# Optimization experiments

Measured on AMD Instinct MI355X. Metric: run time of the kernel, lower is better.

The kernel has to match this reference:

```python
import jax, jax.numpy as jnp
import numpy as np

B, S, J, L, E, H, NI, NT = 8, 32, 4, 32, 500, 500, 5000, 48


def _lstm_scan(x, h0, c0, Wi, Wh, b):
    # x: [T, ..., E]; torch LSTM gate order i,f,g,o
    def step(carry, xt):
        h, c = carry
        z = xt @ Wi.T + h @ Wh.T + b
        i, f, g, o = jnp.split(z, 4, axis=-1)
        c = jax.nn.sigmoid(f) * c + jax.nn.sigmoid(i) * jnp.tanh(g)
        h = jax.nn.sigmoid(o) * jnp.tanh(c)
        return (h, c), h
    (h, c), hs = jax.lax.scan(step, (h0, c0), x)
    return hs, (h, c)


def setup_inputs() -> dict:
    key = jax.random.key(0)
    ks = jax.random.split(key, 24)
    p = lambda k, shp: jax.random.normal(k, shp, jnp.float32) * 0.05
    t = jnp.arange(S)
    return dict(
        item_vectors=jax.random.randint(ks[0], (B, S), 0, NI),
        sequence_tim=jax.random.randint(ks[1], (B, S), 0, NT),
        dilated_idx=jax.random.randint(ks[2], (B, S), 0, S) % jnp.maximum(t, 1)[None, :],
        hist_items=jax.random.randint(ks[3], (B, J, L), 0, NI),
        hist_tims=jax.random.randint(ks[4], (B, J, L), 0, NT),
        mask=jnp.ones((B, S), jnp.float32),
        tim_sim=jax.random.uniform(ks[5], (NT, NT)),
        poi_dist=jax.random.uniform(ks[6], (NI, NI)) + 0.1,
        emb_W=p(ks[7], (NI, E)),
        lstm_Wi=p(ks[8], (4 * H, E)), lstm_Wh=p(ks[9], (4 * H, H)), lstm_b=jnp.zeros((4 * H,)),
        hist_Wi=p(ks[10], (4 * H, E)), hist_Wh=p(ks[11], (4 * H, H)), hist_b=jnp.zeros((4 * H,)),
        dil_Wi=p(ks[12], (4 * H, E)), dil_Wh=p(ks[13], (4 * H, H)), dil_b=jnp.zeros((4 * H,)),
        lin1_W=p(ks[14], (H, H)), lin1_b=jnp.zeros((H,)),
        lin_W=p(ks[15], (NI, 2 * H)), lin_b=jnp.zeros((NI,)),
    )


def _fwd(item_vectors, sequence_tim, dilated_idx, hist_items, hist_tims, mask,
         tim_sim, poi_dist, emb_W, lstm_Wi, lstm_Wh, lstm_b, hist_Wi, hist_Wh,
         hist_b, dil_Wi, dil_Wh, dil_b, lin1_W, lin1_b, lin_W, lin_b):
    items = emb_W[item_vectors]                                  # [B,S,E]
    hs, _ = _lstm_scan(items.transpose(1, 0, 2), jnp.zeros((B, H)), jnp.zeros((B, H)),
                       lstm_Wi, lstm_Wh, lstm_b)
    out = hs.transpose(1, 0, 2)                                  # [B,S,H]

    def dilated_one(xb, idx):
        # dilated LSTMCell: prev state gathered from data-dependent index (zeros at t=0)
        def step(carry, inp):
            Hs, Cs = carry
            t, it, xt = inp
            ph = jnp.where(t == 0, jnp.zeros((H,)), Hs[it])
            pc = jnp.where(t == 0, jnp.zeros((H,)), Cs[it])
            z = xt @ dil_Wi.T + ph @ dil_Wh.T + dil_b
            i, f, g, o = jnp.split(z, 4)
            c = jax.nn.sigmoid(f) * pc + jax.nn.sigmoid(i) * jnp.tanh(g)
            h = jax.nn.sigmoid(o) * jnp.tanh(c)
            return (Hs.at[t].set(h), Cs.at[t].set(c)), None
        (Hs, _), _ = jax.lax.scan(step, (jnp.zeros((S, H)), jnp.zeros((S, H))),
                                  (jnp.arange(S), idx, xb))
        return Hs
    out_hie = jax.vmap(dilated_one)(items, dilated_idx)          # [B,S,H]

    # train-branch session representation: masked mean, same at every step
    denom = jnp.sum(mask, axis=1, keepdims=True)
    pooled = jnp.sum(out * mask[:, :, None], axis=1) / denom     # [B,H]
    csr = jnp.broadcast_to(pooled[:, None, :], (B, S - 1, H))

    def hist_one(items_j, tims_j, timid, poiid, csr_b, out_b):
        jac_rows = tim_sim[timid]                                # [S-1,NT]
        dist_rows = poi_dist[poiid]                              # [S-1,NI]
        def sess_step(carry, inp):
            h2, c2 = carry
            itms, tms = inp
            he, (h2, c2) = _lstm_scan(emb_W[itms], h2, c2, hist_Wi, hist_Wh, hist_b)
            w = jax.nn.softmax(jac_rows[:, tms], axis=1)         # [S-1,L]
            sess_rep = w @ he                                    # [S-1,H]
            avg_d = jnp.mean(dist_rows[:, itms], axis=1)         # [S-1]
            return (h2, c2), (sess_rep, avg_d)
        _, (sess, avgd) = jax.lax.scan(sess_step, (jnp.zeros((H,)), jnp.zeros((H,))),
                                       (items_j, tims_j))
        sess_t = sess.transpose(1, 0, 2)                         # [S-1,J,H]
        avgd_t = avgd.T                                          # [S-1,J]
        sims = jax.nn.softmax(jnp.einsum('sjh,sh->sj', sess_t, csr_b), axis=1)
        out_y = jax.nn.selu(jnp.einsum('sj,sjh->sh', sims, sess_t) @ lin1_W.T + lin1_b)
        layer2 = 0.5 * out_y + 0.5 * out_b[:S - 1]
        l2s = jax.nn.softmax(jnp.einsum('sjh,sh->sj', sess_t, layer2) / avgd_t, axis=1)
        ol2 = jnp.einsum('sj,sjh->sh', l2s, sess_t)              # [S-1,H]
        return jnp.concatenate([ol2, jnp.zeros((1, H))], axis=0)  # pad to [S,H]

    y = jax.nn.selu(jax.vmap(hist_one)(hist_items, hist_tims, sequence_tim[:, :S - 1],
                                       item_vectors[:, :S - 1], csr, out))
    out_mix = 0.5 * (jax.nn.selu(out) + jax.nn.selu(out_hie))
    logits = jnp.concatenate([y, out_mix], axis=2) @ lin_W.T + lin_b
    return jax.nn.log_softmax(logits, axis=-1)


def reference(item_vectors, sequence_tim, dilated_idx, hist_items, hist_tims, mask,
              tim_sim, poi_dist, emb_W, lstm_Wi, lstm_Wh, lstm_b, hist_Wi, hist_Wh,
              hist_b, dil_Wi, dil_Wh, dil_b, lin1_W, lin1_b, lin_W, lin_b):
    return _fwd(item_vectors, sequence_tim, dilated_idx, hist_items, hist_tims, mask,
                tim_sim, poi_dist, emb_W, lstm_Wi, lstm_Wh, lstm_b, hist_Wi, hist_Wh,
                hist_b, dil_Wi, dil_Wh, dil_b, lin1_W, lin1_b, lin_W, lin_b)
```

## Files before the change

### kernel.cpp

```cpp
#include <hip/hip_runtime.h>
#include <hip/hip_bf16.h>
#include <math.h>

#define B_ 8
#define S_ 32
#define J_ 4
#define L_ 32
#define E_ 500
#define H_ 500
#define NI_ 5000
#define NT_ 48
#define G4_ 2000

#define PZH_ 2.0f
#define PZC_ 1e30f

typedef unsigned long long ull;

__device__ __forceinline__ float sigm(float x) { return 1.f / (1.f + expf(-x)); }
__device__ __forceinline__ float seluf(float x) {
    const float sc = 1.0507009873554805f, al = 1.6732632423543772f;
    return x > 0.f ? sc * x : sc * al * (expf(x) - 1.f);
}
__device__ __forceinline__ float cohload(const float* p) {
    return __hip_atomic_load(p, __ATOMIC_RELAXED, __HIP_MEMORY_SCOPE_AGENT);
}
__device__ __forceinline__ ull cohload64(const ull* p) {
    return __hip_atomic_load(p, __ATOMIC_RELAXED, __HIP_MEMORY_SCOPE_AGENT);
}
__device__ __forceinline__ void cohstore(float* p, float v) {
    __hip_atomic_store(p, v, __ATOMIC_RELAXED, __HIP_MEMORY_SCOPE_AGENT);
}

__global__ __launch_bounds__(256) void k_poison(float* __restrict__ outm,
                                                float* __restrict__ outh,
                                                float* __restrict__ csg,
                                                float* __restrict__ he) {
    int i = blockIdx.x * 256 + threadIdx.x;
    if (i < 128000) { outm[i] = PZH_; outh[i] = PZH_; csg[i] = PZC_; }
    if (i < 512000) he[i] = PZH_;
}

__global__ __launch_bounds__(128) void k_embed(const int* __restrict__ itemv,
                                               const int* __restrict__ histi,
                                               const float* __restrict__ embW,
                                               float* __restrict__ items,
                                               float* __restrict__ histemb) {
    int row = blockIdx.x;
    int id;
    float* dst;
    if (row < 256) { id = itemv[row]; dst = items + (size_t)row * E_; }
    else           { int rr = row - 256; id = histi[rr]; dst = histemb + (size_t)rr * E_; }
    const float4* s = (const float4*)(embW + (size_t)id * E_);
    float4* d = (float4*)dst;
    if (threadIdx.x < 125) d[threadIdx.x] = s[threadIdx.x];
}

#define TBM 64
#define TBN 64
#define TBK 16
__global__ __launch_bounds__(256) void k_gemm_bt(const float* __restrict__ A,
                                                 const float* __restrict__ Bm,
                                                 const float* __restrict__ bias,
                                                 float* __restrict__ C,
                                                 int M, int N, int K) {
    __shared__ float As[TBK][TBM + 1];
    __shared__ float Bs[TBK][TBN + 1];
    const int tid = threadIdx.x;
    const int tx = tid & 15, ty = tid >> 4;
    const int row0 = blockIdx.y * TBM, col0 = blockIdx.x * TBN;
    float acc[4][4] = {};
    for (int k0 = 0; k0 < K; k0 += TBK) {
#pragma unroll
        for (int i = 0; i < 4; ++i) {
            int e = tid + i * 256;
            int kk = e & 15, m = e >> 4;
            int gk = k0 + kk;
            float va = 0.f, vb = 0.f;
            int gm = row0 + m, gn = col0 + m;
            if (gk < K) {
                if (gm < M) va = A[(size_t)gm * K + gk];
                if (gn < N) vb = Bm[(size_t)gn * K + gk];
            }
            As[kk][m] = va;
            Bs[kk][m] = vb;
        }
        __syncthreads();
#pragma unroll
        for (int kk = 0; kk < TBK; ++kk) {
            float a[4], bb[4];
#pragma unroll
            for (int i = 0; i < 4; ++i) a[i] = As[kk][ty * 4 + i];
#pragma unroll
            for (int i = 0; i < 4; ++i) bb[i] = Bs[kk][tx * 4 + i];
#pragma unroll
            for (int i = 0; i < 4; ++i)
#pragma unroll
                for (int j = 0; j < 4; ++j) acc[i][j] += a[i] * bb[j];
        }
        __syncthreads();
    }
#pragma unroll
    for (int i = 0; i < 4; ++i) {
        int gm = row0 + ty * 4 + i;
        if (gm >= M) continue;
#pragma unroll
        for (int j = 0; j < 4; ++j) {
            int gn = col0 + tx * 4 + j;
            if (gn < N) C[(size_t)gm * N + gn] = acc[i][j] + (bias ? bias[gn] : 0.f);
        }
    }
}

__global__ __launch_bounds__(256) void k_rec10(
    const float* __restrict__ xwm, const float* __restrict__ Whm,
    const float* __restrict__ xwd, const float* __restrict__ Whd,
    const int* __restrict__ dilidx,
    const float* __restrict__ xwh, const float* __restrict__ Whh,
    float* __restrict__ outm, float* __restrict__ outh,
    float* __restrict__ csg, float* __restrict__ he) {
    __shared__ __align__(16) float4 h_s4[125];
    __shared__ float z_s[256];
    const int tid = threadIdx.x;
    const int bid = blockIdx.x;
    const int x = bid & 7, ii = bid >> 3;
    int role, b, blk;
    if (x < 4)      { role = 2; b = x * 2 + (ii >> 4);       blk = ii & 15; }
    else if (x < 6) { role = 0; b = (x - 4) * 4 + (ii >> 3); blk = ii & 7;  }
    else            { role = 1; b = (x - 6) * 4 + (ii >> 3); blk = ii & 7;  }

    const int hpbb   = (role == 2) ? 32 : 63;
    const int r0     = blk * hpbb;
    const int hpb    = min(hpbb, 500 - r0);
    const int C      = 4 * hpb;
    const int nsteps = (role == 2) ? 128 : 32;

    const float* Wh = (role == 0) ? Whm : (role == 1) ? Whd : Whh;
    const float* xw = (role == 0) ? xwm : (role == 1) ? xwd : xwh;

    int colg = 0;
    if (tid < C) {
        int gate = tid / hpb;
        int ri = tid - gate * hpb;
        colg = gate * 500 + r0 + ri;
    }
    const float4* wp4 = (const float4*)(Wh + (size_t)colg * 500);

    float c_reg = 0.f;

    for (int t = 0; t < nsteps; ++t) {
        float acc = 0.f;
        if (tid < C) acc = xw[((size_t)(b * nsteps + t)) * G4_ + colg];

        float pc_r = 0.f;
        if (t > 0) {
            const float* hrow;
            if (role == 0)      hrow = outm + ((size_t)(b * S_ + (t - 1))) * H_;
            else if (role == 2) hrow = he + ((size_t)(b * 128 + (t - 1))) * H_;
            else { int it = dilidx[b * S_ + t];
                   hrow = outh + ((size_t)(b * S_ + it)) * H_; }
            if (tid < 125) {
                const ull* p = (const ull*)(hrow + tid * 4);
                union { ull u[2]; float4 f; float fs[4]; } uf;
                while (true) {
                    uf.u[0] = cohload64(p);
                    uf.u[1] = cohload64(p + 1);
                    if (uf.fs[0] != PZH_ && uf.fs[1] != PZH_ &&
                        uf.fs[2] != PZH_ && uf.fs[3] != PZH_) break;
                    __builtin_amdgcn_s_sleep(1);
                }
                h_s4[tid] = uf.f;
            }
            if (role == 1 && tid < hpb) {
                int it = dilidx[b * S_ + t];
                const float* pp = &csg[((size_t)(b * S_ + it)) * H_ + r0 + tid];
                do { pc_r = cohload(pp); } while (pc_r == PZC_);
            }
            __syncthreads();

            if (tid < C) {
                float s0 = 0.f, s1 = 0.f, s2 = 0.f, s3 = 0.f;
#pragma unroll 2
                for (int k4 = 0; k4 < 124; k4 += 4) {
                    float4 w0 = wp4[k4],     h0 = h_s4[k4];
                    float4 w1 = wp4[k4 + 1], h1 = h_s4[k4 + 1];
                    float4 w2 = wp4[k4 + 2], h2 = h_s4[k4 + 2];
                    float4 w3 = wp4[k4 + 3], h3 = h_s4[k4 + 3];
                    s0 += w0.x * h0.x + w0.y * h0.y + w0.z * h0.z + w0.w * h0.w;
                    s1 += w1.x * h1.x + w1.y * h1.y + w1.z * h1.z + w1.w * h1.w;
                    s2 += w2.x * h2.x + w2.y * h2.y + w2.z * h2.z + w2.w * h2.w;
                    s3 += w3.x * h3.x + w3.y * h3.y + w3.z * h3.z + w3.w * h3.w;
                }
                float4 wt = wp4[124], ht = h_s4[124];
                s0 += wt.x * ht.x + wt.y * ht.y + wt.z * ht.z + wt.w * ht.w;
                acc += (s0 + s1) + (s2 + s3);
            }
        }
        z_s[tid] = acc;
        __syncthreads();

        if (tid < hpb) {
            float zi = z_s[tid];
            float zf = z_s[tid + hpb];
            float zg = z_s[tid + 2 * hpb];
            float zo = z_s[tid + 3 * hpb];
            float pc = (role == 1) ? pc_r : c_reg;
            float cc = sigm(zf) * pc + sigm(zi) * tanhf(zg);
            float hh = sigm(zo) * tanhf(cc);
            c_reg = cc;
            int r = r0 + tid;
            if (role == 0) {
                cohstore(&outm[((size_t)(b * S_ + t)) * H_ + r], hh);
            } else if (role == 2) {
                cohstore(&he[((size_t)(b * 128 + t)) * H_ + r], hh);
            } else {
                cohstore(&outh[((size_t)(b * S_ + t)) * H_ + r], hh);
                cohstore(&csg[((size_t)(b * S_ + t)) * H_ + r], cc);
            }
        }
        __syncthreads();
    }
}

__global__ __launch_bounds__(512) void k_pool(const float* __restrict__ outm,
                                              const float* __restrict__ mask,
                                              float* __restrict__ pooled) {
    int b = blockIdx.x, tid = threadIdx.x;
    if (tid >= 500) return;
    float acc = 0.f, den = 0.f;
    for (int s = 0; s < S_; ++s) {
        float mk = mask[b * S_ + s];
        acc += outm[((size_t)(b * S_ + s)) * H_ + tid] * mk;
        den += mk;
    }
    pooled[b * H_ + tid] = acc / den;
}

__global__ __launch_bounds__(512) void k_sess(const int* __restrict__ seqtim,
                                              const int* __restrict__ itemv,
                                              const int* __restrict__ histt,
                                              const int* __restrict__ histi,
                                              const float* __restrict__ timsim,
                                              const float* __restrict__ poid,
                                              const float* __restrict__ he,
                                              float* __restrict__ sess,
                                              float* __restrict__ avgd) {
    int bi = blockIdx.x;
    int s = bi % 31;
    int tmpv = bi / 31;
    int j = tmpv & 3, b = tmpv >> 2;
    __shared__ float w[L_];
    __shared__ float pd[L_];
    __shared__ float stats[1];
    int tid = threadIdx.x;
    int st = seqtim[b * S_ + s];
    if (tid < L_) {
        int ht = histt[(b * J_ + j) * L_ + tid];
        w[tid] = timsim[st * NT_ + ht];
    }
    if (tid >= 64 && tid < 64 + L_) {
        int l = tid - 64;
        int iv = itemv[b * S_ + s];
        pd[l] = poid[(size_t)iv * NI_ + histi[(b * J_ + j) * L_ + l]];
    }
    __syncthreads();
    if (tid == 64) {
        float a = 0.f;
        for (int l = 0; l < L_; ++l) a += pd[l];
        avgd[(b * J_ + j) * 31 + s] = a * (1.f / 32.f);
    }
    if (tid == 0) {
        float m = -1e30f;
        for (int l = 0; l < L_; ++l) m = fmaxf(m, w[l]);
        float sm = 0.f;
        for (int l = 0; l < L_; ++l) { float e = expf(w[l] - m); w[l] = e; sm += e; }
        stats[0] = 1.f / sm;
    }
    __syncthreads();
    if (tid < 500) {
        float inv = stats[0];
        float acc = 0.f;
        const float* hp = he + ((size_t)(b * J_ * L_ + j * L_)) * H_ + tid;
        for (int l = 0; l < L_; ++l) acc += w[l] * inv * hp[(size_t)l * H_];
        sess[((size_t)((b * J_ + j) * 31 + s)) * H_ + tid] = acc;
    }
}

__global__ __launch_bounds__(512) void k_att1(const float* __restrict__ sess,
                                              const float* __restrict__ pooled,
                                              float* __restrict__ att1) {
    int bi = blockIdx.x;
    int s = bi % 31, b = bi / 31;
    __shared__ float vec[H_];
    __shared__ float part[512];
    int tid = threadIdx.x;
    if (tid < 500) vec[tid] = pooled[b * H_ + tid];
    __syncthreads();
    int j = tid >> 7, i = tid & 127;
    const float* sp = sess + ((size_t)((b * J_ + j) * 31 + s)) * H_;
    float acc = 0.f;
    for (int h = i; h < H_; h += 128) acc += sp[h] * vec[h];
    part[tid] = acc;
    __syncthreads();
    for (int off = 64; off > 0; off >>= 1) {
        if (i < off) part[tid] += part[tid + off];
        __syncthreads();
    }
    float d0 = part[0], d1 = part[128], d2 = part[256], d3 = part[384];
    float m = fmaxf(fmaxf(d0, d1), fmaxf(d2, d3));
    float e0 = expf(d0 - m), e1 = expf(d1 - m), e2 = expf(d2 - m), e3 = expf(d3 - m);
    float inv = 1.f / (e0 + e1 + e2 + e3);
    if (tid < 500) {
        const float* s0 = sess + ((size_t)(b * J_ * 31 + s)) * H_ + tid;
        const size_t js = (size_t)31 * H_;
        float r = e0 * inv * s0[0] + e1 * inv * s0[js] + e2 * inv * s0[2 * js] + e3 * inv * s0[3 * js];
        att1[((size_t)(b * 31 + s)) * H_ + tid] = r;
    }
}

__global__ __launch_bounds__(512) void k_att2(const float* __restrict__ sess,
                                              const float* __restrict__ outy,
                                              const float* __restrict__ outm,
                                              const float* __restrict__ avgd,
                                              float* __restrict__ X) {
    int bi = blockIdx.x;
    int s = bi % 31, b = bi / 31;
    __shared__ float vec[H_];
    __shared__ float part[512];
    int tid = threadIdx.x;
    if (tid < 500)
        vec[tid] = 0.5f * seluf(outy[((size_t)(b * 31 + s)) * H_ + tid]) +
                   0.5f * outm[((size_t)(b * S_ + s)) * H_ + tid];
    __syncthreads();
    int j = tid >> 7, i = tid & 127;
    const float* sp = sess + ((size_t)((b * J_ + j) * 31 + s)) * H_;
    float acc = 0.f;
    for (int h = i; h < H_; h += 128) acc += sp[h] * vec[h];
    part[tid] = acc;
    __syncthreads();
    for (int off = 64; off > 0; off >>= 1) {
        if (i < off) part[tid] += part[tid + off];
        __syncthreads();
    }
    float d0 = part[0]   / avgd[(b * J_ + 0) * 31 + s];
    float d1 = part[128] / avgd[(b * J_ + 1) * 31 + s];
    float d2 = part[256] / avgd[(b * J_ + 2) * 31 + s];
    float d3 = part[384] / avgd[(b * J_ + 3) * 31 + s];
    float m = fmaxf(fmaxf(d0, d1), fmaxf(d2, d3));
    float e0 = expf(d0 - m), e1 = expf(d1 - m), e2 = expf(d2 - m), e3 = expf(d3 - m);
    float inv = 1.f / (e0 + e1 + e2 + e3);
    if (tid < 500) {
        const float* s0 = sess + ((size_t)(b * J_ * 31 + s)) * H_ + tid;
        const size_t js = (size_t)31 * H_;
        float r = e0 * inv * s0[0] + e1 * inv * s0[js] + e2 * inv * s0[2 * js] + e3 * inv * s0[3 * js];
        X[((size_t)(b * S_ + s)) * 1000 + tid] = seluf(r);
    }
}

__global__ __launch_bounds__(512) void k_mix(const float* __restrict__ outm,
                                             const float* __restrict__ outh,
                                             float* __restrict__ X) {
    int bs = blockIdx.x;
    int tid = threadIdx.x;
    if (tid >= 500) return;
    size_t idx = (size_t)bs * H_ + tid;
    float om = 0.5f * (seluf(outm[idx]) + seluf(outh[idx]));
    X[(size_t)bs * 1000 + 500 + tid] = om;
    if ((bs & (S_ - 1)) == S_ - 1) X[(size_t)bs * 1000 + tid] = 0.f;
}

__global__ __launch_bounds__(512) void k_lsm(float* __restrict__ out) {
    int row = blockIdx.x, tid = threadIdx.x;
    float* p = out + (size_t)row * NI_;
    __shared__ float red[512];
    float m = -1e30f;
    for (int i = tid; i < NI_; i += 512) m = fmaxf(m, p[i]);
    red[tid] = m;
    __syncthreads();
    for (int off = 256; off > 0; off >>= 1) {
        if (tid < off) red[tid] = fmaxf(red[tid], red[tid + off]);
        __syncthreads();
    }
    m = red[0];
    __syncthreads();
    float sm = 0.f;
    for (int i = tid; i < NI_; i += 512) sm += expf(p[i] - m);
    red[tid] = sm;
    __syncthreads();
    for (int off = 256; off > 0; off >>= 1) {
        if (tid < off) red[tid] += red[tid + off];
        __syncthreads();
    }
    float lse = m + logf(red[0]);
    __syncthreads();
    for (int i = tid; i < NI_; i += 512) p[i] -= lse;
}

extern "C" void kernel_launch(void* const* d_in, const int* in_sizes, int n_in,
                              void* d_out, int out_size, void* d_ws, size_t ws_size,
                              hipStream_t stream) {
    const int* item_vectors = (const int*)d_in[0];
    const int* sequence_tim = (const int*)d_in[1];
    const int* dilated_idx  = (const int*)d_in[2];
    const int* hist_items   = (const int*)d_in[3];
    const int* hist_tims    = (const int*)d_in[4];
    const float* mask       = (const float*)d_in[5];
    const float* tim_sim    = (const float*)d_in[6];
    const float* poi_dist   = (const float*)d_in[7];
    const float* emb_W      = (const float*)d_in[8];
    const float* lstm_Wi    = (const float*)d_in[9];
    const float* lstm_Wh    = (const float*)d_in[10];
    const float* lstm_b     = (const float*)d_in[11];
    const float* hist_Wi    = (const float*)d_in[12];
    const float* hist_Wh    = (const float*)d_in[13];
    const float* hist_b     = (const float*)d_in[14];
    const float* dil_Wi     = (const float*)d_in[15];
    const float* dil_Wh     = (const float*)d_in[16];
    const float* dil_b      = (const float*)d_in[17];
    const float* lin1_W     = (const float*)d_in[18];
    const float* lin1_b     = (const float*)d_in[19];
    const float* lin_W      = (const float*)d_in[20];
    const float* lin_b      = (const float*)d_in[21];
    float* out = (float*)d_out;
    float* ws  = (float*)d_ws;

    float* items   = ws + 0;
    float* histemb = ws + 128000;
    float* xwm     = ws + 640000;
    float* xwd     = ws + 1152000;
    float* xwh     = ws + 1664000;
    float* outm    = ws + 3712000;
    float* outh    = ws + 3840000;
    float* csg     = ws + 3968000;
    float* he      = ws + 4096000;
    float* pooled  = ws + 4608000;
    float* sess    = ws + 4612000;
    float* avgd    = ws + 5108000;
    float* att1    = ws + 5108992;
    float* outy    = ws + 5232992;
    float* Xbuf    = ws + 5356992;

    k_poison<<<dim3(2000), dim3(256), 0, stream>>>(outm, outh, csg, he);
    k_embed<<<dim3(1280), dim3(128), 0, stream>>>(item_vectors, hist_items, emb_W, items, histemb);

    k_gemm_bt<<<dim3(32, 4), dim3(256), 0, stream>>>(items, lstm_Wi, lstm_b, xwm, 256, G4_, E_);
    k_gemm_bt<<<dim3(32, 4), dim3(256), 0, stream>>>(items, dil_Wi, dil_b, xwd, 256, G4_, E_);
    k_gemm_bt<<<dim3(32, 16), dim3(256), 0, stream>>>(histemb, hist_Wi, hist_b, xwh, 1024, G4_, E_);

    k_rec10<<<dim3(256), dim3(256), 0, stream>>>(
        xwm, lstm_Wh, xwd, dil_Wh, dilated_idx, xwh, hist_Wh,
        outm, outh, csg, he);

    k_pool<<<dim3(B_), dim3(512), 0, stream>>>(outm, mask, pooled);
    k_sess<<<dim3(B_ * J_ * 31), dim3(512), 0, stream>>>(sequence_tim, item_vectors, hist_tims,
                                                         hist_items, tim_sim, poi_dist, he, sess, avgd);
    k_att1<<<dim3(B_ * 31), dim3(512), 0, stream>>>(sess, pooled, att1);
    k_gemm_bt<<<dim3(8, 4), dim3(256), 0, stream>>>(att1, lin1_W, lin1_b, outy, 248, H_, H_);
    k_att2<<<dim3(B_ * 31), dim3(512), 0, stream>>>(sess, outy, outm, avgd, Xbuf);
    k_mix<<<dim3(B_ * S_), dim3(512), 0, stream>>>(outm, outh, Xbuf);

    k_gemm_bt<<<dim3(79, 4), dim3(256), 0, stream>>>(Xbuf, lin_W, lin_b, out, 256, NI_, 1000);
    k_lsm<<<dim3(256), dim3(512), 0, stream>>>(out);
}
```

Baseline: 1.892 ms.

## Fuse embedding gather into input GEMMs, replace poison kernel with memset, merge mix into att2

Swaps the poison kernel for a single hipMemsetAsync that fills the sync buffers with a 0x7F7F7F7F bit pattern, and the recurrence now spin-waits on that bit pattern. Folds the embedding gather into a single three-way batched input-projection GEMM launch, so the items/histemb buffers are never materialized. Also folds the mix kernel into the att2 kernel, which now covers all 32 steps. Together these cut launch count and intermediate memory traffic. In exchange the GEMM does an indirect embedding load per A element, and blocks in the z=0/1 slices whose rows lie past 256 exit early.

```diff
diff --git a/kernel.cpp b/kernel.cpp
--- a/kernel.cpp
+++ b/kernel.cpp
@@ -12,8 +12,7 @@
 #define NT_ 48
 #define G4_ 2000
 
-#define PZH_ 2.0f
-#define PZC_ 1e30f
+#define PZBITS_ 0x7F7F7F7Fu
 
 typedef unsigned long long ull;
 
@@ -32,33 +31,72 @@
     __hip_atomic_store(p, v, __ATOMIC_RELAXED, __HIP_MEMORY_SCOPE_AGENT);
 }
 
-__global__ __launch_bounds__(256) void k_poison(float* __restrict__ outm,
-                                                float* __restrict__ outh,
-                                                float* __restrict__ csg,
-                                                float* __restrict__ he) {
-    int i = blockIdx.x * 256 + threadIdx.x;
-    if (i < 128000) { outm[i] = PZH_; outh[i] = PZH_; csg[i] = PZC_; }
-    if (i < 512000) he[i] = PZH_;
-}
-
-__global__ __launch_bounds__(128) void k_embed(const int* __restrict__ itemv,
-                                               const int* __restrict__ histi,
-                                               const float* __restrict__ embW,
-                                               float* __restrict__ items,
-                                               float* __restrict__ histemb) {
-    int row = blockIdx.x;
-    int id;
-    float* dst;
-    if (row < 256) { id = itemv[row]; dst = items + (size_t)row * E_; }
-    else           { int rr = row - 256; id = histi[rr]; dst = histemb + (size_t)rr * E_; }
-    const float4* s = (const float4*)(embW + (size_t)id * E_);
-    float4* d = (float4*)dst;
-    if (threadIdx.x < 125) d[threadIdx.x] = s[threadIdx.x];
-}
-
 #define TBM 64
 #define TBN 64
 #define TBK 16
+__global__ __launch_bounds__(256) void k_gemm_emb(
+    const int* __restrict__ itemv, const int* __restrict__ histi,
+    const float* __restrict__ embW,
+    const float* __restrict__ Wm, const float* __restrict__ bm, float* __restrict__ Cm,
+    const float* __restrict__ Wd, const float* __restrict__ bd, float* __restrict__ Cd,
+    const float* __restrict__ Wh, const float* __restrict__ bh, float* __restrict__ Ch) {
+    const int z = blockIdx.z;
+    int M; const int* idx; const float* Bm; const float* bias; float* C;
+    if (z == 0)      { M = 256;  idx = itemv; Bm = Wm; bias = bm; C = Cm; }
+    else if (z == 1) { M = 256;  idx = itemv; Bm = Wd; bias = bd; C = Cd; }
+    else             { M = 1024; idx = histi; Bm = Wh; bias = bh; C = Ch; }
+    const int row0 = blockIdx.y * TBM;
+    if (row0 >= M) return;
+    const int col0 = blockIdx.x * TBN;
+    const int K = E_, N = G4_;
+
+    __shared__ float As[TBK][TBM + 1];
+    __shared__ float Bs[TBK][TBN + 1];
+    const int tid = threadIdx.x;
+    const int tx = tid & 15, ty = tid >> 4;
+    float acc[4][4] = {};
+    for (int k0 = 0; k0 < K; k0 += TBK) {
+#pragma unroll
+        for (int i = 0; i < 4; ++i) {
+            int e = tid + i * 256;
+            int kk = e & 15, m = e >> 4;
+            int gk = k0 + kk;
+            float va = 0.f, vb = 0.f;
+            int gm = row0 + m, gn = col0 + m;
+            if (gk < K) {
+                if (gm < M) va = embW[(size_t)idx[gm] * E_ + gk];
+                if (gn < N) vb = Bm[(size_t)gn * K + gk];
+            }
+            As[kk][m] = va;
+            Bs[kk][m] = vb;
+        }
+        __syncthreads();
+#pragma unroll
+        for (int kk = 0; kk < TBK; ++kk) {
+            float a[4], bb[4];
+#pragma unroll
+            for (int i = 0; i < 4; ++i) a[i] = As[kk][ty * 4 + i];
+#pragma unroll
+            for (int i = 0; i < 4; ++i) bb[i] = Bs[kk][tx * 4 + i];
+#pragma unroll
+            for (int i = 0; i < 4; ++i)
+#pragma unroll
+                for (int j = 0; j < 4; ++j) acc[i][j] += a[i] * bb[j];
+        }
+        __syncthreads();
+    }
+#pragma unroll
+    for (int i = 0; i < 4; ++i) {
+        int gm = row0 + ty * 4 + i;
+        if (gm >= M) continue;
+#pragma unroll
+        for (int j = 0; j < 4; ++j) {
+            int gn = col0 + tx * 4 + j;
+            if (gn < N) C[(size_t)gm * N + gn] = acc[i][j] + bias[gn];
+        }
+    }
+}
+
 __global__ __launch_bounds__(256) void k_gemm_bt(const float* __restrict__ A,
                                                  const float* __restrict__ Bm,
                                                  const float* __restrict__ bias,
@@ -112,7 +150,7 @@
     }
 }
 
-__global__ __launch_bounds__(256) void k_rec10(
+__global__ __launch_bounds__(256) void k_rec12(
     const float* __restrict__ xwm, const float* __restrict__ Whm,
     const float* __restrict__ xwd, const float* __restrict__ Whd,
     const int* __restrict__ dilidx,
@@ -161,12 +199,12 @@
                    hrow = outh + ((size_t)(b * S_ + it)) * H_; }
             if (tid < 125) {
                 const ull* p = (const ull*)(hrow + tid * 4);
-                union { ull u[2]; float4 f; float fs[4]; } uf;
+                union { ull u[2]; float4 f; unsigned us[4]; } uf;
                 while (true) {
                     uf.u[0] = cohload64(p);
                     uf.u[1] = cohload64(p + 1);
-                    if (uf.fs[0] != PZH_ && uf.fs[1] != PZH_ &&
-                        uf.fs[2] != PZH_ && uf.fs[3] != PZH_) break;
+                    if (uf.us[0] != PZBITS_ && uf.us[1] != PZBITS_ &&
+                        uf.us[2] != PZBITS_ && uf.us[3] != PZBITS_) break;
                     __builtin_amdgcn_s_sleep(1);
                 }
                 h_s4[tid] = uf.f;
@@ -174,7 +212,7 @@
             if (role == 1 && tid < hpb) {
                 int it = dilidx[b * S_ + t];
                 const float* pp = &csg[((size_t)(b * S_ + it)) * H_ + r0 + tid];
-                do { pc_r = cohload(pp); } while (pc_r == PZC_);
+                do { pc_r = cohload(pp); } while (__float_as_uint(pc_r) == PZBITS_);
             }
             __syncthreads();
 
@@ -318,16 +356,28 @@
     }
 }
 
-__global__ __launch_bounds__(512) void k_att2(const float* __restrict__ sess,
-                                              const float* __restrict__ outy,
-                                              const float* __restrict__ outm,
-                                              const float* __restrict__ avgd,
-                                              float* __restrict__ X) {
+__global__ __launch_bounds__(512) void k_att2m(const float* __restrict__ sess,
+                                               const float* __restrict__ outy,
+                                               const float* __restrict__ outm,
+                                               const float* __restrict__ outh,
+                                               const float* __restrict__ avgd,
+                                               float* __restrict__ X) {
     int bi = blockIdx.x;
-    int s = bi % 31, b = bi / 31;
+    int s = bi & 31, b = bi >> 5;
+    int tid = threadIdx.x;
     __shared__ float vec[H_];
     __shared__ float part[512];
-    int tid = threadIdx.x;
+
+    if (tid < 500) {
+        size_t idx = (size_t)(b * S_ + s) * H_ + tid;
+        X[(size_t)(b * S_ + s) * 1000 + 500 + tid] =
+            0.5f * (seluf(outm[idx]) + seluf(outh[idx]));
+    }
+    if (s == 31) {
+        if (tid < 500) X[(size_t)(b * S_ + s) * 1000 + tid] = 0.f;
+        return;
+    }
+
     if (tid < 500)
         vec[tid] = 0.5f * seluf(outy[((size_t)(b * 31 + s)) * H_ + tid]) +
                    0.5f * outm[((size_t)(b * S_ + s)) * H_ + tid];
@@ -355,18 +405,6 @@
         float r = e0 * inv * s0[0] + e1 * inv * s0[js] + e2 * inv * s0[2 * js] + e3 * inv * s0[3 * js];
         X[((size_t)(b * S_ + s)) * 1000 + tid] = seluf(r);
     }
-}
-
-__global__ __launch_bounds__(512) void k_mix(const float* __restrict__ outm,
-                                             const float* __restrict__ outh,
-                                             float* __restrict__ X) {
-    int bs = blockIdx.x;
-    int tid = threadIdx.x;
-    if (tid >= 500) return;
-    size_t idx = (size_t)bs * H_ + tid;
-    float om = 0.5f * (seluf(outm[idx]) + seluf(outh[idx]));
-    X[(size_t)bs * 1000 + 500 + tid] = om;
-    if ((bs & (S_ - 1)) == S_ - 1) X[(size_t)bs * 1000 + tid] = 0.f;
 }
 
 __global__ __launch_bounds__(512) void k_lsm(float* __restrict__ out) {
@@ -424,8 +462,6 @@
     float* out = (float*)d_out;
     float* ws  = (float*)d_ws;
 
-    float* items   = ws + 0;
-    float* histemb = ws + 128000;
     float* xwm     = ws + 640000;
     float* xwd     = ws + 1152000;
     float* xwh     = ws + 1664000;
@@ -440,14 +476,15 @@
     float* outy    = ws + 5232992;
     float* Xbuf    = ws + 5356992;
 
-    k_poison<<<dim3(2000), dim3(256), 0, stream>>>(outm, outh, csg, he);
-    k_embed<<<dim3(1280), dim3(128), 0, stream>>>(item_vectors, hist_items, emb_W, items, histemb);
-
-    k_gemm_bt<<<dim3(32, 4), dim3(256), 0, stream>>>(items, lstm_Wi, lstm_b, xwm, 256, G4_, E_);
-    k_gemm_bt<<<dim3(32, 4), dim3(256), 0, stream>>>(items, dil_Wi, dil_b, xwd, 256, G4_, E_);
-    k_gemm_bt<<<dim3(32, 16), dim3(256), 0, stream>>>(histemb, hist_Wi, hist_b, xwh, 1024, G4_, E_);
-
-    k_rec10<<<dim3(256), dim3(256), 0, stream>>>(
+    hipMemsetAsync((void*)outm, 0x7F, (size_t)896000 * sizeof(float), stream);
+
+    k_gemm_emb<<<dim3(32, 16, 3), dim3(256), 0, stream>>>(
+        item_vectors, hist_items, emb_W,
+        lstm_Wi, lstm_b, xwm,
+        dil_Wi,  dil_b,  xwd,
+        hist_Wi, hist_b, xwh);
+
+    k_rec12<<<dim3(256), dim3(256), 0, stream>>>(
         xwm, lstm_Wh, xwd, dil_Wh, dilated_idx, xwh, hist_Wh,
         outm, outh, csg, he);
 
@@ -456,8 +493,7 @@
                                                          hist_items, tim_sim, poi_dist, he, sess, avgd);
     k_att1<<<dim3(B_ * 31), dim3(512), 0, stream>>>(sess, pooled, att1);
     k_gemm_bt<<<dim3(8, 4), dim3(256), 0, stream>>>(att1, lin1_W, lin1_b, outy, 248, H_, H_);
-    k_att2<<<dim3(B_ * 31), dim3(512), 0, stream>>>(sess, outy, outm, avgd, Xbuf);
-    k_mix<<<dim3(B_ * S_), dim3(512), 0, stream>>>(outm, outh, Xbuf);
+    k_att2m<<<dim3(B_ * 32), dim3(512), 0, stream>>>(sess, outy, outm, outh, avgd, Xbuf);
 
     k_gemm_bt<<<dim3(79, 4), dim3(256), 0, stream>>>(Xbuf, lin_W, lin_b, out, 256, NI_, 1000);
     k_lsm<<<dim3(256), dim3(512), 0, stream>>>(out);
```

After: 1.742 ms. -7.9%, faster.
